# Kernel optimization log

Hardware: AMD Instinct MI355X
Metric: run time of the kernel (lower is better)

Reference implementation:

```python
import jax, jax.numpy as jnp
import numpy as np

B, T, D, H, DFF = 2, 2048, 1024, 16, 4096
DK = D // H
EPS = 1e-5


def setup_inputs() -> dict:
    key = jax.random.key(0)
    ks = jax.random.split(key, 8)
    s = 0.02
    return {
        "x": jax.random.normal(ks[0], (B, T, D), jnp.float32),
        "Wq": jax.random.normal(ks[1], (D, D), jnp.float32) * s,
        "Wk": jax.random.normal(ks[2], (D, D), jnp.float32) * s,
        "Wv": jax.random.normal(ks[3], (D, D), jnp.float32) * s,
        "Wo": jax.random.normal(ks[4], (D, D), jnp.float32) * s,
        "W1": jax.random.normal(ks[5], (DFF, D), jnp.float32) * s,
        "b1": jnp.zeros((DFF,), jnp.float32),
        "W2": jax.random.normal(ks[6], (DFF, DFF), jnp.float32) * s,
        "b2": jnp.zeros((DFF,), jnp.float32),
        "W3": jax.random.normal(ks[7], (D, DFF), jnp.float32) * s,
        "b3": jnp.zeros((D,), jnp.float32),
        "gamma1": jnp.ones((D,), jnp.float32),
        "beta1": jnp.zeros((D,), jnp.float32),
        "gamma2": jnp.ones((D,), jnp.float32),
        "beta2": jnp.zeros((D,), jnp.float32),
    }


def _layernorm(X, gamma, beta):
    X = X.astype(jnp.float32)
    mean = X.mean(axis=-1, keepdims=True)
    var = X.var(axis=-1, keepdims=True)  # unbiased=False
    X_hat = (X - mean) * jax.lax.rsqrt(var + EPS)
    return gamma * X_hat + beta


def _block(x, Wq, Wk, Wv, Wo, W1, b1, W2, b2, W3, b3, gamma1, beta1, gamma2, beta2):
    Bx, Tx, _ = x.shape
    # attention (nn.Linear: y = x @ W.T)
    Q = (x @ Wq.T).reshape(Bx, Tx, H, DK).transpose(0, 2, 1, 3)  # (B,H,T,dk)
    K = (x @ Wk.T).reshape(Bx, Tx, H, DK).transpose(0, 2, 1, 3)
    V = (x @ Wv.T).reshape(Bx, Tx, H, DK).transpose(0, 2, 1, 3)
    scores = jnp.einsum("bhqd,bhkd->bhqk", Q, K) / jnp.sqrt(jnp.float32(DK))
    causal = jnp.tril(jnp.ones((Tx, Tx), bool))
    scores = jnp.where(causal, scores, -jnp.inf)
    attn = jax.nn.softmax(scores.astype(jnp.float32), axis=-1)
    out = jnp.einsum("bhqk,bhkd->bhqd", attn, V)
    out = out.transpose(0, 2, 1, 3).reshape(Bx, Tx, D)
    attention = out @ Wo.T
    # addnorm1 (dropout=0)
    x = _layernorm(attention + x, gamma1, beta1)
    # FFN: 3 linears with exact GELU
    h = jax.nn.gelu(x @ W1.T + b1, approximate=False)
    h = jax.nn.gelu(h @ W2.T + b2, approximate=False)
    ffn_out = h @ W3.T + b3
    # addnorm2
    return _layernorm(ffn_out + x, gamma2, beta2)


def reference(x, Wq, Wk, Wv, Wo, W1, b1, W2, b2, W3, b3, gamma1, beta1, gamma2, beta2):
    return _block(x, Wq, Wk, Wv, Wo, W1, b1, W2, b2, W3, b3, gamma1, beta1, gamma2, beta2)
```

## Files before the change

### kernel.cpp

```cpp
#include <hip/hip_runtime.h>
#include <hip/hip_bf16.h>


#define B_   2
#define T_   2048
#define D_   1024
#define H_   16
#define DK_  64
#define DFF_ 4096
#define M_   (B_ * T_)

using short8 = __attribute__((ext_vector_type(8))) short;
using f32x4  = __attribute__((ext_vector_type(4))) float;
using us4    = __attribute__((ext_vector_type(4))) unsigned short;

__device__ __forceinline__ unsigned short f2bf(float f) {
  unsigned u = __float_as_uint(f);
  u += 0x7FFFu + ((u >> 16) & 1u);
  return (unsigned short)(u >> 16);
}

#define GLDS16(g, l)                                                      \
  __builtin_amdgcn_global_load_lds(                                       \
      (const __attribute__((address_space(1))) unsigned int*)(g),         \
      (__attribute__((address_space(3))) unsigned int*)(l), 16, 0, 0)

__global__ __launch_bounds__(256) void f2bf_k(const float* __restrict__ in,
                                              unsigned short* __restrict__ out,
                                              int n4) {
  int i = blockIdx.x * 256 + threadIdx.x;
  const int stride = gridDim.x * 256;
  for (; i < n4; i += stride) {
    const float4 v = ((const float4*)in)[i];
    us4 o;
    o[0] = f2bf(v.x); o[1] = f2bf(v.y); o[2] = f2bf(v.z); o[3] = f2bf(v.w);
    ((us4*)out)[i] = o;
  }
}

template <int MODE>
__global__ __launch_bounds__(256) void gemm_bt(
    const unsigned short* __restrict__ A, const unsigned short* __restrict__ Bw,
    const float* __restrict__ bias, const float* __restrict__ res,
    void* __restrict__ outp, int N, int K) {
  __shared__ unsigned short lA[128 * 32];
  __shared__ unsigned short lB[128 * 32];
  const int tid  = threadIdx.x;
  const int lane = tid & 63;
  const int wave = tid >> 6;
  const int row0 = blockIdx.y << 7;
  const int col0 = blockIdx.x << 7;
  const int wr = (wave >> 1) << 6;
  const int wc = (wave & 1) << 6;
  const int r  = lane & 15;
  const int c8 = (lane >> 4) << 3;

  const f32x4 z4 = {0.f, 0.f, 0.f, 0.f};
  f32x4 acc[4][4];
#pragma unroll
  for (int m = 0; m < 4; ++m)
#pragma unroll
    for (int n = 0; n < 4; ++n) acc[m][n] = z4;

  const unsigned short* gA = A + (size_t)(row0 + (tid >> 2)) * K + (tid & 3) * 8;
  const unsigned short* gB = Bw + (size_t)(col0 + (tid >> 2)) * K + (tid & 3) * 8;
  const size_t rstep = (size_t)64 * K;
  unsigned short* lAd = lA + tid * 8;
  unsigned short* lBd = lB + tid * 8;

  for (int kt = 0; kt < K; kt += 32) {
    GLDS16(gA + kt,         lAd);
    GLDS16(gA + kt + rstep, lAd + 2048);
    GLDS16(gB + kt,         lBd);
    GLDS16(gB + kt + rstep, lBd + 2048);
    __syncthreads();
    short8 af[4], bf[4];
#pragma unroll
    for (int m = 0; m < 4; ++m)
      af[m] = *(const short8*)&lA[(wr + m * 16 + r) * 32 + c8];
#pragma unroll
    for (int n = 0; n < 4; ++n)
      bf[n] = *(const short8*)&lB[(wc + n * 16 + r) * 32 + c8];
#pragma unroll
    for (int m = 0; m < 4; ++m)
#pragma unroll
      for (int n = 0; n < 4; ++n)
        acc[m][n] = __builtin_amdgcn_mfma_f32_16x16x32_bf16(af[m], bf[n],
                                                            acc[m][n], 0, 0, 0);
    __syncthreads();
  }

#pragma unroll
  for (int m = 0; m < 4; ++m) {
    const int gr0 = row0 + wr + m * 16 + ((lane >> 4) << 2);
#pragma unroll
    for (int n = 0; n < 4; ++n) {
      const int gc = col0 + wc + n * 16 + r;
#pragma unroll
      for (int j = 0; j < 4; ++j) {
        const int gr = gr0 + j;
        float v = acc[m][n][j];
        if (MODE == 0) {
          const int b = gr >> 11, t = gr & (T_ - 1);
          const int h = gc >> 6, d = gc & 63;
          ((unsigned short*)outp)[(((size_t)(b * H_ + h) * T_ + t) << 6) + d] =
              f2bf(v);
        } else if (MODE == 1) {
          const size_t o = (size_t)gr * N + gc;
          ((float*)outp)[o] = v + res[o];
        } else if (MODE == 2) {
          float xv = v + bias[gc];
          float g  = 0.5f * xv * (1.f + erff(xv * 0.70710678118654752f));
          ((unsigned short*)outp)[(size_t)gr * N + gc] = f2bf(g);
        } else {
          const size_t o = (size_t)gr * N + gc;
          ((float*)outp)[o] = v + bias[gc] + res[o];
        }
      }
    }
  }
}

__device__ __forceinline__ int swzK(int row, int col) {
  return row * 64 + (col ^ ((row & 7) << 3));
}
__device__ __forceinline__ int swzV(int row, int col) {
  return row * 64 + (col ^ (((row ^ (row >> 3)) & 7) << 3));
}

__global__ __launch_bounds__(256) void attn_k(
    const unsigned short* __restrict__ Q, const unsigned short* __restrict__ Kp,
    const unsigned short* __restrict__ Vp, unsigned short* __restrict__ O) {
  const int bh = blockIdx.y;
  const int qt = gridDim.x - 1 - blockIdx.x;
  const int q0 = qt << 6;
  const size_t base = (size_t)bh * T_ * DK_;
  const unsigned short* Qb = Q + base;
  const unsigned short* Kb = Kp + base;
  const unsigned short* Vb = Vp + base;
  const int tid = threadIdx.x, lane = tid & 63, wave = tid >> 6;
  const int r = lane & 15, c8 = (lane >> 4) << 3;

  __shared__ unsigned short lK[64 * 64];
  __shared__ unsigned short lV[64 * 64];
  __shared__ unsigned short lP[64 * 64];

  const short8 qf0 = *(const short8*)&Qb[(size_t)(q0 + wave * 16 + r) * 64 + c8];
  const short8 qf1 = *(const short8*)&Qb[(size_t)(q0 + wave * 16 + r) * 64 + 32 + c8];

  const f32x4 z4 = {0.f, 0.f, 0.f, 0.f};
  f32x4 o[4];
#pragma unroll
  for (int n = 0; n < 4; ++n) o[n] = z4;
  float mrow[4], lrow[4];
#pragma unroll
  for (int j = 0; j < 4; ++j) { mrow[j] = -1e30f; lrow[j] = 0.f; }

  const int kr = tid >> 3;
  const int kc = ((tid & 7) * 8) ^ ((kr & 7) << 3);
  const int vc = (tid & 7) * 8;

  for (int kt = 0; kt <= qt; ++kt) {
    __syncthreads();
    GLDS16(&Kb[((size_t)kt * 64 + kr) * 64 + kc],      lK + tid * 8);
    GLDS16(&Kb[((size_t)kt * 64 + 32 + kr) * 64 + kc], lK + 2048 + tid * 8);
    const short8 v0 = *(const short8*)&Vb[((size_t)kt * 64 + kr) * 64 + vc];
    const short8 v1 = *(const short8*)&Vb[((size_t)kt * 64 + 32 + kr) * 64 + vc];
#pragma unroll
    for (int e = 0; e < 8; ++e) {
      const int d0 = vc + e;
      lV[swzV(d0, kr)]      = (unsigned short)v0[e];
      lV[swzV(d0, kr + 32)] = (unsigned short)v1[e];
    }
    __syncthreads();

    f32x4 s[4];
#pragma unroll
    for (int n = 0; n < 4; ++n) {
      const int krow = n * 16 + r;
      const short8 k0 = *(const short8*)&lK[swzK(krow, c8)];
      const short8 k1 = *(const short8*)&lK[swzK(krow, c8 + 32)];
      f32x4 z = z4;
      z = __builtin_amdgcn_mfma_f32_16x16x32_bf16(qf0, k0, z, 0, 0, 0);
      z = __builtin_amdgcn_mfma_f32_16x16x32_bf16(qf1, k1, z, 0, 0, 0);
      s[n] = z;
    }

    const bool diag = (kt == qt);
#pragma unroll
    for (int n = 0; n < 4; ++n)
#pragma unroll
      for (int j = 0; j < 4; ++j) {
        float sv = s[n][j] * 0.125f;
        if (diag) {
          const int kk = n * 16 + r;
          const int qq = wave * 16 + ((lane >> 4) << 2) + j;
          if (kk > qq) sv = -1e30f;
        }
        s[n][j] = sv;
      }

#pragma unroll
    for (int j = 0; j < 4; ++j) {
      float mx = fmaxf(fmaxf(s[0][j], s[1][j]), fmaxf(s[2][j], s[3][j]));
#pragma unroll
      for (int msk = 1; msk < 16; msk <<= 1) mx = fmaxf(mx, __shfl_xor(mx, msk));
      const float mnew = fmaxf(mrow[j], mx);
      const float c = __expf(mrow[j] - mnew);
      mrow[j] = mnew;
      float rs = 0.f;
#pragma unroll
      for (int n = 0; n < 4; ++n) {
        const float p = __expf(s[n][j] - mnew);
        s[n][j] = p;
        rs += p;
      }
#pragma unroll
      for (int msk = 1; msk < 16; msk <<= 1) rs += __shfl_xor(rs, msk);
      lrow[j] = lrow[j] * c + rs;
#pragma unroll
      for (int n = 0; n < 4; ++n) o[n][j] *= c;
    }

#pragma unroll
    for (int n = 0; n < 4; ++n)
#pragma unroll
      for (int j = 0; j < 4; ++j) {
        const int q  = ((lane >> 4) << 2) + j;
        const int kk = n * 16 + r;
        lP[wave * 1024 + swzK(q, kk)] = f2bf(s[n][j]);
      }
    asm volatile("s_waitcnt lgkmcnt(0)" ::: "memory");

    const short8 pa0 = *(const short8*)&lP[wave * 1024 + swzK(r, c8)];
    const short8 pa1 = *(const short8*)&lP[wave * 1024 + swzK(r, c8 + 32)];
#pragma unroll
    for (int n = 0; n < 4; ++n) {
      const int dr = n * 16 + r;
      const short8 vb0 = *(const short8*)&lV[swzV(dr, c8)];
      const short8 vb1 = *(const short8*)&lV[swzV(dr, c8 + 32)];
      o[n] = __builtin_amdgcn_mfma_f32_16x16x32_bf16(pa0, vb0, o[n], 0, 0, 0);
      o[n] = __builtin_amdgcn_mfma_f32_16x16x32_bf16(pa1, vb1, o[n], 0, 0, 0);
    }
  }

  const int b = bh >> 4, h = bh & 15;
  float rinv[4];
#pragma unroll
  for (int j = 0; j < 4; ++j) rinv[j] = 1.f / lrow[j];
#pragma unroll
  for (int n = 0; n < 4; ++n)
#pragma unroll
    for (int j = 0; j < 4; ++j) {
      const int q = q0 + wave * 16 + ((lane >> 4) << 2) + j;
      const int d = n * 16 + r;
      O[((size_t)(b * T_ + q) * D_) + h * 64 + d] = f2bf(o[n][j] * rinv[j]);
    }
}

__global__ __launch_bounds__(256) void ln_k(const float* __restrict__ in,
                                            const float* __restrict__ gam,
                                            const float* __restrict__ bet,
                                            float* __restrict__ o32,
                                            unsigned short* __restrict__ obf) {
  const int row = blockIdx.x;
  const int tid = threadIdx.x, lane = tid & 63, wave = tid >> 6;
  const float4 v = ((const float4*)(in + (size_t)row * D_))[tid];
  __shared__ float sm[8];
  float s = v.x + v.y + v.z + v.w;
#pragma unroll
  for (int m = 32; m >= 1; m >>= 1) s += __shfl_xor(s, m);
  if (lane == 0) sm[wave] = s;
  __syncthreads();
  const float mean = (sm[0] + sm[1] + sm[2] + sm[3]) * (1.f / 1024.f);
  const float dx = v.x - mean, dy = v.y - mean, dz = v.z - mean, dw = v.w - mean;
  float q = dx * dx + dy * dy + dz * dz + dw * dw;
#pragma unroll
  for (int m = 32; m >= 1; m >>= 1) q += __shfl_xor(q, m);
  if (lane == 0) sm[4 + wave] = q;
  __syncthreads();
  const float var = (sm[4] + sm[5] + sm[6] + sm[7]) * (1.f / 1024.f);
  const float inv = rsqrtf(var + 1e-5f);
  const float4 g = ((const float4*)gam)[tid];
  const float4 b = ((const float4*)bet)[tid];
  float4 y;
  y.x = dx * inv * g.x + b.x;
  y.y = dy * inv * g.y + b.y;
  y.z = dz * inv * g.z + b.z;
  y.w = dw * inv * g.w + b.w;
  ((float4*)(o32 + (size_t)row * D_))[tid] = y;
  if (obf) {
    us4 o;
    o[0] = f2bf(y.x); o[1] = f2bf(y.y); o[2] = f2bf(y.z); o[3] = f2bf(y.w);
    ((us4*)(obf + (size_t)row * D_))[tid] = o;
  }
}

#define MB(x) ((size_t)(x) << 20)

extern "C" void kernel_launch(void* const* d_in, const int* in_sizes, int n_in,
                              void* d_out, int out_size, void* d_ws,
                              size_t ws_size, hipStream_t stream) {
  const float* x   = (const float*)d_in[0];
  const float* Wq  = (const float*)d_in[1];
  const float* Wk  = (const float*)d_in[2];
  const float* Wv  = (const float*)d_in[3];
  const float* Wo  = (const float*)d_in[4];
  const float* W1  = (const float*)d_in[5];
  const float* b1  = (const float*)d_in[6];
  const float* W2  = (const float*)d_in[7];
  const float* b2  = (const float*)d_in[8];
  const float* W3  = (const float*)d_in[9];
  const float* b3  = (const float*)d_in[10];
  const float* g1  = (const float*)d_in[11];
  const float* be1 = (const float*)d_in[12];
  const float* g2  = (const float*)d_in[13];
  const float* be2 = (const float*)d_in[14];
  float* out = (float*)d_out;

  char* w = (char*)d_ws;
  unsigned short* Wq_bf = (unsigned short*)(w + MB(0));
  unsigned short* Wk_bf = (unsigned short*)(w + MB(2));
  unsigned short* Wv_bf = (unsigned short*)(w + MB(4));
  unsigned short* Wo_bf = (unsigned short*)(w + MB(6));
  unsigned short* W1_bf = (unsigned short*)(w + MB(8));
  unsigned short* W2_bf = (unsigned short*)(w + MB(16));
  unsigned short* W3_bf = (unsigned short*)(w + MB(48));
  unsigned short* x_bf  = (unsigned short*)(w + MB(56));
  unsigned short* q_bf  = (unsigned short*)(w + MB(64));
  unsigned short* k_bf  = (unsigned short*)(w + MB(72));
  unsigned short* v_bf  = (unsigned short*)(w + MB(80));
  unsigned short* a_bf  = (unsigned short*)(w + MB(88));
  float*          res1  = (float*)(w + MB(96));
  float*          ln1f  = (float*)(w + MB(120));
  unsigned short* ln1bf = (unsigned short*)(w + MB(136));
  unsigned short* h1_bf = (unsigned short*)(w + MB(56));
  unsigned short* h2_bf = (unsigned short*)(w + MB(88));
  float*          res2  = (float*)(w + MB(56));

  auto cvt = [&](const float* src, unsigned short* dst, int n) {
    const int n4 = n >> 2;
    int blocks = (n4 + 255) / 256;
    if (blocks > 2048) blocks = 2048;
    f2bf_k<<<dim3(blocks), dim3(256), 0, stream>>>(src, dst, n4);
  };
  cvt(x,  x_bf,  M_ * D_);
  cvt(Wq, Wq_bf, D_ * D_);
  cvt(Wk, Wk_bf, D_ * D_);
  cvt(Wv, Wv_bf, D_ * D_);
  cvt(Wo, Wo_bf, D_ * D_);
  cvt(W1, W1_bf, DFF_ * D_);
  cvt(W2, W2_bf, DFF_ * DFF_);
  cvt(W3, W3_bf, D_ * DFF_);

  const dim3 blk(256);
  const dim3 gD(D_ / 128, M_ / 128);
  const dim3 gF(DFF_ / 128, M_ / 128);

  gemm_bt<0><<<gD, blk, 0, stream>>>(x_bf, Wq_bf, nullptr, nullptr, q_bf, D_, D_);
  gemm_bt<0><<<gD, blk, 0, stream>>>(x_bf, Wk_bf, nullptr, nullptr, k_bf, D_, D_);
  gemm_bt<0><<<gD, blk, 0, stream>>>(x_bf, Wv_bf, nullptr, nullptr, v_bf, D_, D_);

  attn_k<<<dim3(T_ / 64, B_ * H_), blk, 0, stream>>>(q_bf, k_bf, v_bf, a_bf);

  gemm_bt<1><<<gD, blk, 0, stream>>>(a_bf, Wo_bf, nullptr, x, res1, D_, D_);
  ln_k<<<dim3(M_), blk, 0, stream>>>(res1, g1, be1, ln1f, ln1bf);

  gemm_bt<2><<<gF, blk, 0, stream>>>(ln1bf, W1_bf, b1, nullptr, h1_bf, DFF_, D_);
  gemm_bt<2><<<gF, blk, 0, stream>>>(h1_bf, W2_bf, b2, nullptr, h2_bf, DFF_, DFF_);
  gemm_bt<3><<<gD, blk, 0, stream>>>(h2_bf, W3_bf, b3, ln1f, res2, D_, DFF_);

  ln_k<<<dim3(M_), blk, 0, stream>>>(res2, g2, be2, out, nullptr);
}
```

Baseline: 811.2 us.

## Rewrite GEMMs with 256x256 pipelined tiles, fuse QKV, split-K W3, widen attention tiles

Most of the pipeline is replaced. The eight conversion launches become one kernel, and Q/K/V are fused into a single GEMM over concatenated weights. The FFN GEMMs move to a new 512-thread 256x256-tile kernel that double-buffers LDS and uses explicit waitcnt, barriers and priority scheduling. The W3 GEMM is split along K into four partial buffers that a separate kernel sums together with bias and residual. Attention now processes 128-key tiles and uses exp2 with a prescaled log2e factor, cutting loop iterations and barrier overhead at the cost of more LDS and extra partial-sum memory traffic.

```diff
diff --git a/kernel.cpp b/kernel.cpp
--- a/kernel.cpp
+++ b/kernel.cpp
@@ -19,59 +19,221 @@
   u += 0x7FFFu + ((u >> 16) & 1u);
   return (unsigned short)(u >> 16);
 }
+__device__ __forceinline__ us4 pack4(float4 v) {
+  us4 o; o[0] = f2bf(v.x); o[1] = f2bf(v.y); o[2] = f2bf(v.z); o[3] = f2bf(v.w);
+  return o;
+}
 
 #define GLDS16(g, l)                                                      \
   __builtin_amdgcn_global_load_lds(                                       \
       (const __attribute__((address_space(1))) unsigned int*)(g),         \
       (__attribute__((address_space(3))) unsigned int*)(l), 16, 0, 0)
 
-__global__ __launch_bounds__(256) void f2bf_k(const float* __restrict__ in,
-                                              unsigned short* __restrict__ out,
-                                              int n4) {
+#define SB   __builtin_amdgcn_s_barrier()
+#define LG0  do { asm volatile("s_waitcnt lgkmcnt(0)" ::: "memory"); \
+                  __builtin_amdgcn_sched_barrier(0); } while (0)
+#define VMW2 do { asm volatile("s_waitcnt vmcnt(2)" ::: "memory");   \
+                  __builtin_amdgcn_sched_barrier(0); } while (0)
+#define VMW0 do { asm volatile("s_waitcnt vmcnt(0)" ::: "memory");   \
+                  __builtin_amdgcn_sched_barrier(0); } while (0)
+#define PR1  __builtin_amdgcn_s_setprio(1)
+#define PR0  __builtin_amdgcn_s_setprio(0)
+
+__global__ __launch_bounds__(256) void cvt_all(
+    const float* __restrict__ x,  const float* __restrict__ wq,
+    const float* __restrict__ wk, const float* __restrict__ wv,
+    const float* __restrict__ wo, const float* __restrict__ w1,
+    const float* __restrict__ w2, const float* __restrict__ w3,
+    us4* __restrict__ xb, us4* __restrict__ qkvw, us4* __restrict__ wob,
+    us4* __restrict__ w1b, us4* __restrict__ w2b, us4* __restrict__ w3b) {
   int i = blockIdx.x * 256 + threadIdx.x;
   const int stride = gridDim.x * 256;
-  for (; i < n4; i += stride) {
-    const float4 v = ((const float4*)in)[i];
-    us4 o;
-    o[0] = f2bf(v.x); o[1] = f2bf(v.y); o[2] = f2bf(v.z); o[3] = f2bf(v.w);
-    ((us4*)out)[i] = o;
+  for (; i < 8388608; i += stride) {
+    const float4* s; us4* d; int off;
+    if      (i < 1048576) { s = (const float4*)x;  d = xb;            off = i; }
+    else if (i < 1310720) { s = (const float4*)wq; d = qkvw;          off = i - 1048576; }
+    else if (i < 1572864) { s = (const float4*)wk; d = qkvw + 262144; off = i - 1310720; }
+    else if (i < 1835008) { s = (const float4*)wv; d = qkvw + 524288; off = i - 1572864; }
+    else if (i < 2097152) { s = (const float4*)wo; d = wob;           off = i - 1835008; }
+    else if (i < 3145728) { s = (const float4*)w1; d = w1b;           off = i - 2097152; }
+    else if (i < 7340032) { s = (const float4*)w2; d = w2b;           off = i - 3145728; }
+    else                  { s = (const float4*)w3; d = w3b;           off = i - 7340032; }
+    d[off] = pack4(s[off]);
   }
 }
 
 template <int MODE>
+__global__ __launch_bounds__(512, 2) void gemm8p(
+    const unsigned short* __restrict__ A, const unsigned short* __restrict__ Bw,
+    const float* __restrict__ bias, unsigned short* __restrict__ oq,
+    unsigned short* __restrict__ ok, unsigned short* __restrict__ ov,
+    float* __restrict__ pLo, float* __restrict__ pHi,
+    int N, int ldk, int klen) {
+  extern __shared__ unsigned short sm[];
+  unsigned short* lA = sm;
+  unsigned short* lB = sm + 32768;
+  const int tid = threadIdx.x, lane = tid & 63, w = tid >> 6;
+  const int wm = w >> 2, wn = w & 3;
+  const int wnlo = (wn & 1) * 64, wnhi = wn >> 1;
+  const int r16 = lane & 15, c8a = (lane >> 4) << 3;
+  const int row0 = blockIdx.y << 8, col0 = blockIdx.x << 8;
+  const int kb = (MODE == 4) ? blockIdx.z * klen : 0;
+
+  const int srow = tid >> 3;
+  const int scol = ((tid & 7) * 8) ^ ((srow & 7) << 3);
+  const size_t off0 = (size_t)srow * ldk + scol;
+  const size_t off1 = (size_t)(srow + 64) * ldk + scol;
+
+  auto stA = [&](int kt, int h) {
+    const unsigned short* g =
+        A + (size_t)(row0 + h * 128) * ldk + kb + (size_t)kt * 64;
+    unsigned short* d = lA + ((kt & 1) * 2 + h) * 8192;
+    GLDS16(g + off0, d + tid * 8);
+    GLDS16(g + off1, d + 4096 + tid * 8);
+  };
+  auto stB = [&](int kt, int h) {
+    const unsigned short* g =
+        Bw + (size_t)(col0 + h * 128) * ldk + kb + (size_t)kt * 64;
+    unsigned short* d = lB + ((kt & 1) * 2 + h) * 8192;
+    GLDS16(g + off0, d + tid * 8);
+    GLDS16(g + off1, d + 4096 + tid * 8);
+  };
+
+  f32x4 acc[8][4];
+#pragma unroll
+  for (int m = 0; m < 8; ++m)
+#pragma unroll
+    for (int n = 0; n < 4; ++n) acc[m][n] = (f32x4){0.f, 0.f, 0.f, 0.f};
+
+  short8 aR[4][2], bR[2][2];
+
+#define LDA4(DB, MQ)                                                         \
+  do {                                                                       \
+    _Pragma("unroll") for (int mf_ = 0; mf_ < 4; ++mf_) {                    \
+      const int rr = (MQ)*64 + mf_ * 16 + r16;                               \
+      const int bb = ((DB)*2 + wm) * 8192 + rr * 64;                         \
+      const int sw = (rr & 7) << 3;                                          \
+      aR[mf_][0] = *(const short8*)&lA[bb + (c8a ^ sw)];                     \
+      aR[mf_][1] = *(const short8*)&lA[bb + ((c8a + 32) ^ sw)];              \
+    }                                                                        \
+  } while (0)
+#define LDB2(DB, NP)                                                         \
+  do {                                                                       \
+    _Pragma("unroll") for (int nf_ = 0; nf_ < 2; ++nf_) {                    \
+      const int rr = wnlo + ((NP)*2 + nf_) * 16 + r16;                       \
+      const int bb = ((DB)*2 + wnhi) * 8192 + rr * 64;                       \
+      const int sw = (rr & 7) << 3;                                          \
+      bR[nf_][0] = *(const short8*)&lB[bb + (c8a ^ sw)];                     \
+      bR[nf_][1] = *(const short8*)&lB[bb + ((c8a + 32) ^ sw)];              \
+    }                                                                        \
+  } while (0)
+#define MMQ(MQ, NP)                                                          \
+  do {                                                                       \
+    _Pragma("unroll") for (int mf_ = 0; mf_ < 4; ++mf_)                      \
+    _Pragma("unroll") for (int nf_ = 0; nf_ < 2; ++nf_) {                    \
+      f32x4 c_ = acc[(MQ)*4 + mf_][(NP)*2 + nf_];                            \
+      c_ = __builtin_amdgcn_mfma_f32_16x16x32_bf16(aR[mf_][0], bR[nf_][0],   \
+                                                   c_, 0, 0, 0);             \
+      c_ = __builtin_amdgcn_mfma_f32_16x16x32_bf16(aR[mf_][1], bR[nf_][1],   \
+                                                   c_, 0, 0, 0);             \
+      acc[(MQ)*4 + mf_][(NP)*2 + nf_] = c_;                                  \
+    }                                                                        \
+  } while (0)
+#define TAIL(MQ, NP) SB; LG0; PR1; MMQ(MQ, NP); PR0; SB
+
+  const int nkt = klen >> 6;
+  stA(0, 0); stA(0, 1); stB(0, 0); stB(0, 1);
+
+  for (int i = 0; i < nkt; i += 2) {
+    stA(i + 1, 0);
+    VMW2;
+    SB;
+    LDA4(0, 0); LDB2(0, 0);
+    TAIL(0, 0);
+    stA(i + 1, 1);
+    LDB2(0, 1);
+    TAIL(0, 1);
+    stB(i + 1, 0);
+    LDA4(0, 1);
+    TAIL(1, 1);
+    stB(i + 1, 1);
+    LDB2(0, 0);
+    TAIL(1, 0);
+    const bool more = (i + 2 < nkt);
+    if (more) { stA(i + 2, 0); VMW2; } else { VMW0; }
+    SB;
+    LDA4(1, 0); LDB2(1, 0);
+    TAIL(0, 0);
+    if (more) stA(i + 2, 1);
+    LDB2(1, 1);
+    TAIL(0, 1);
+    if (more) stB(i + 2, 0);
+    LDA4(1, 1);
+    TAIL(1, 1);
+    if (more) stB(i + 2, 1);
+    LDB2(1, 0);
+    TAIL(1, 0);
+  }
+
+#pragma unroll
+  for (int am = 0; am < 8; ++am) {
+    const int gr0 = row0 + wm * 128 + am * 16 + ((lane >> 4) << 2);
+#pragma unroll
+    for (int an = 0; an < 4; ++an) {
+      const int gc = col0 + wn * 64 + an * 16 + r16;
+#pragma unroll
+      for (int j = 0; j < 4; ++j) {
+        const int gr = gr0 + j;
+        float v = acc[am][an][j];
+        if (MODE == 0) {
+          const int which = gc >> 10, c1 = gc & 1023;
+          const int b = gr >> 11, t = gr & (T_ - 1);
+          const int h = c1 >> 6, d = c1 & 63;
+          unsigned short* dst = (which == 0) ? oq : (which == 1) ? ok : ov;
+          dst[(((size_t)(b * H_ + h) * T_ + t) << 6) + d] = f2bf(v);
+        } else if (MODE == 2) {
+          float xv = v + bias[gc];
+          float g  = 0.5f * xv * (1.f + erff(xv * 0.70710678118654752f));
+          oq[(size_t)gr * N + gc] = f2bf(g);
+        } else {
+          const int z = blockIdx.z;
+          float* o = (z < 2) ? pLo + (size_t)z * (M_ * 1024)
+                             : pHi + (size_t)(z - 2) * (M_ * 1024);
+          o[(size_t)gr * 1024 + gc] = v;
+        }
+      }
+    }
+  }
+#undef LDA4
+#undef LDB2
+#undef MMQ
+#undef TAIL
+}
+
 __global__ __launch_bounds__(256) void gemm_bt(
     const unsigned short* __restrict__ A, const unsigned short* __restrict__ Bw,
-    const float* __restrict__ bias, const float* __restrict__ res,
-    void* __restrict__ outp, int N, int K) {
+    const float* __restrict__ res, float* __restrict__ outp, int N, int K) {
   __shared__ unsigned short lA[128 * 32];
   __shared__ unsigned short lB[128 * 32];
-  const int tid  = threadIdx.x;
-  const int lane = tid & 63;
-  const int wave = tid >> 6;
-  const int row0 = blockIdx.y << 7;
-  const int col0 = blockIdx.x << 7;
-  const int wr = (wave >> 1) << 6;
-  const int wc = (wave & 1) << 6;
-  const int r  = lane & 15;
-  const int c8 = (lane >> 4) << 3;
-
+  const int tid = threadIdx.x, lane = tid & 63, wave = tid >> 6;
+  const int row0 = blockIdx.y << 7, col0 = blockIdx.x << 7;
+  const int wr = (wave >> 1) << 6, wc = (wave & 1) << 6;
+  const int r = lane & 15, c8 = (lane >> 4) << 3;
   const f32x4 z4 = {0.f, 0.f, 0.f, 0.f};
   f32x4 acc[4][4];
 #pragma unroll
   for (int m = 0; m < 4; ++m)
 #pragma unroll
     for (int n = 0; n < 4; ++n) acc[m][n] = z4;
-
   const unsigned short* gA = A + (size_t)(row0 + (tid >> 2)) * K + (tid & 3) * 8;
   const unsigned short* gB = Bw + (size_t)(col0 + (tid >> 2)) * K + (tid & 3) * 8;
   const size_t rstep = (size_t)64 * K;
   unsigned short* lAd = lA + tid * 8;
   unsigned short* lBd = lB + tid * 8;
-
   for (int kt = 0; kt < K; kt += 32) {
-    GLDS16(gA + kt,         lAd);
+    GLDS16(gA + kt, lAd);
     GLDS16(gA + kt + rstep, lAd + 2048);
-    GLDS16(gB + kt,         lBd);
+    GLDS16(gB + kt, lBd);
     GLDS16(gB + kt + rstep, lBd + 2048);
     __syncthreads();
     short8 af[4], bf[4];
@@ -89,7 +251,6 @@
                                                             acc[m][n], 0, 0, 0);
     __syncthreads();
   }
-
 #pragma unroll
   for (int m = 0; m < 4; ++m) {
     const int gr0 = row0 + wr + m * 16 + ((lane >> 4) << 2);
@@ -98,34 +259,11 @@
       const int gc = col0 + wc + n * 16 + r;
 #pragma unroll
       for (int j = 0; j < 4; ++j) {
-        const int gr = gr0 + j;
-        float v = acc[m][n][j];
-        if (MODE == 0) {
-          const int b = gr >> 11, t = gr & (T_ - 1);
-          const int h = gc >> 6, d = gc & 63;
-          ((unsigned short*)outp)[(((size_t)(b * H_ + h) * T_ + t) << 6) + d] =
-              f2bf(v);
-        } else if (MODE == 1) {
-          const size_t o = (size_t)gr * N + gc;
-          ((float*)outp)[o] = v + res[o];
-        } else if (MODE == 2) {
-          float xv = v + bias[gc];
-          float g  = 0.5f * xv * (1.f + erff(xv * 0.70710678118654752f));
-          ((unsigned short*)outp)[(size_t)gr * N + gc] = f2bf(g);
-        } else {
-          const size_t o = (size_t)gr * N + gc;
-          ((float*)outp)[o] = v + bias[gc] + res[o];
-        }
-      }
-    }
-  }
-}
-
-__device__ __forceinline__ int swzK(int row, int col) {
-  return row * 64 + (col ^ ((row & 7) << 3));
-}
-__device__ __forceinline__ int swzV(int row, int col) {
-  return row * 64 + (col ^ (((row ^ (row >> 3)) & 7) << 3));
+        const size_t o = (size_t)(gr0 + j) * N + gc;
+        outp[o] = acc[m][n][j] + res[o];
+      }
+    }
+  }
 }
 
 __global__ __launch_bounds__(256) void attn_k(
@@ -141,12 +279,13 @@
   const int tid = threadIdx.x, lane = tid & 63, wave = tid >> 6;
   const int r = lane & 15, c8 = (lane >> 4) << 3;
 
-  __shared__ unsigned short lK[64 * 64];
-  __shared__ unsigned short lV[64 * 64];
-  __shared__ unsigned short lP[64 * 64];
+  __shared__ unsigned short lK[128 * 64];
+  __shared__ unsigned short lV[64 * 128];
+  __shared__ unsigned short lP[4 * 16 * 128];
 
   const short8 qf0 = *(const short8*)&Qb[(size_t)(q0 + wave * 16 + r) * 64 + c8];
-  const short8 qf1 = *(const short8*)&Qb[(size_t)(q0 + wave * 16 + r) * 64 + 32 + c8];
+  const short8 qf1 =
+      *(const short8*)&Qb[(size_t)(q0 + wave * 16 + r) * 64 + 32 + c8];
 
   const f32x4 z4 = {0.f, 0.f, 0.f, 0.f};
   f32x4 o[4];
@@ -156,63 +295,75 @@
 #pragma unroll
   for (int j = 0; j < 4; ++j) { mrow[j] = -1e30f; lrow[j] = 0.f; }
 
-  const int kr = tid >> 3;
-  const int kc = ((tid & 7) * 8) ^ ((kr & 7) << 3);
-  const int vc = (tid & 7) * 8;
-
-  for (int kt = 0; kt <= qt; ++kt) {
+  const float SCL = 0.125f * 1.44269504088896f;
+  const int krow = tid >> 3;
+  const int kcol = ((tid & 7) * 8) ^ ((krow & 7) << 3);
+
+  const int niter = (q0 >> 7) + 1;
+  for (int kt = 0; kt < niter; ++kt) {
     __syncthreads();
-    GLDS16(&Kb[((size_t)kt * 64 + kr) * 64 + kc],      lK + tid * 8);
-    GLDS16(&Kb[((size_t)kt * 64 + 32 + kr) * 64 + kc], lK + 2048 + tid * 8);
-    const short8 v0 = *(const short8*)&Vb[((size_t)kt * 64 + kr) * 64 + vc];
-    const short8 v1 = *(const short8*)&Vb[((size_t)kt * 64 + 32 + kr) * 64 + vc];
-#pragma unroll
-    for (int e = 0; e < 8; ++e) {
-      const int d0 = vc + e;
-      lV[swzV(d0, kr)]      = (unsigned short)v0[e];
-      lV[swzV(d0, kr + 32)] = (unsigned short)v1[e];
-    }
+    const unsigned short* Kt = Kb + ((size_t)kt << 7) * 64;
+    GLDS16(Kt + krow * 64 + kcol,         lK + tid * 8);
+    GLDS16(Kt + (krow + 32) * 64 + kcol,  lK + 2048 + tid * 8);
+    GLDS16(Kt + (krow + 64) * 64 + kcol,  lK + 4096 + tid * 8);
+    GLDS16(Kt + (krow + 96) * 64 + kcol,  lK + 6144 + tid * 8);
+    const unsigned short* Vt = Vb + ((size_t)kt << 7) * 64;
+    short8 vld[4];
+#pragma unroll
+    for (int l = 0; l < 4; ++l)
+      vld[l] = *(const short8*)&Vt[(size_t)((tid >> 3) + 32 * l) * 64 +
+                                   (tid & 7) * 8];
+#pragma unroll
+    for (int l = 0; l < 4; ++l)
+#pragma unroll
+      for (int e = 0; e < 8; ++e) {
+        const int dd = (tid & 7) * 8 + e, kv = (tid >> 3) + 32 * l;
+        lV[dd * 128 + (kv ^ ((dd & 7) << 3))] = (unsigned short)vld[l][e];
+      }
     __syncthreads();
 
-    f32x4 s[4];
-#pragma unroll
-    for (int n = 0; n < 4; ++n) {
-      const int krow = n * 16 + r;
-      const short8 k0 = *(const short8*)&lK[swzK(krow, c8)];
-      const short8 k1 = *(const short8*)&lK[swzK(krow, c8 + 32)];
+    f32x4 s[8];
+#pragma unroll
+    for (int nf = 0; nf < 8; ++nf) {
+      const int kr = nf * 16 + r;
+      const int sw = (kr & 7) << 3;
+      const short8 k0 = *(const short8*)&lK[kr * 64 + (c8 ^ sw)];
+      const short8 k1 = *(const short8*)&lK[kr * 64 + ((c8 + 32) ^ sw)];
       f32x4 z = z4;
       z = __builtin_amdgcn_mfma_f32_16x16x32_bf16(qf0, k0, z, 0, 0, 0);
       z = __builtin_amdgcn_mfma_f32_16x16x32_bf16(qf1, k1, z, 0, 0, 0);
-      s[n] = z;
-    }
-
-    const bool diag = (kt == qt);
-#pragma unroll
-    for (int n = 0; n < 4; ++n)
+      s[nf] = z;
+    }
+
+    const bool tail = (kt == niter - 1);
+#pragma unroll
+    for (int nf = 0; nf < 8; ++nf)
 #pragma unroll
       for (int j = 0; j < 4; ++j) {
-        float sv = s[n][j] * 0.125f;
-        if (diag) {
-          const int kk = n * 16 + r;
-          const int qq = wave * 16 + ((lane >> 4) << 2) + j;
-          if (kk > qq) sv = -1e30f;
+        float sv = s[nf][j] * SCL;
+        if (tail) {
+          const int kg = (kt << 7) + nf * 16 + r;
+          const int qg = q0 + wave * 16 + ((lane >> 4) << 2) + j;
+          if (kg > qg) sv = -1e30f;
         }
-        s[n][j] = sv;
+        s[nf][j] = sv;
       }
 
 #pragma unroll
     for (int j = 0; j < 4; ++j) {
-      float mx = fmaxf(fmaxf(s[0][j], s[1][j]), fmaxf(s[2][j], s[3][j]));
+      float mx = s[0][j];
+#pragma unroll
+      for (int nf = 1; nf < 8; ++nf) mx = fmaxf(mx, s[nf][j]);
 #pragma unroll
       for (int msk = 1; msk < 16; msk <<= 1) mx = fmaxf(mx, __shfl_xor(mx, msk));
       const float mnew = fmaxf(mrow[j], mx);
-      const float c = __expf(mrow[j] - mnew);
+      const float c = exp2f(mrow[j] - mnew);
       mrow[j] = mnew;
       float rs = 0.f;
 #pragma unroll
-      for (int n = 0; n < 4; ++n) {
-        const float p = __expf(s[n][j] - mnew);
-        s[n][j] = p;
+      for (int nf = 0; nf < 8; ++nf) {
+        const float p = exp2f(s[nf][j] - mnew);
+        s[nf][j] = p;
         rs += p;
       }
 #pragma unroll
@@ -222,25 +373,34 @@
       for (int n = 0; n < 4; ++n) o[n][j] *= c;
     }
 
-#pragma unroll
-    for (int n = 0; n < 4; ++n)
+    unsigned short* Pw = lP + wave * 2048;
+#pragma unroll
+    for (int nf = 0; nf < 8; ++nf)
 #pragma unroll
       for (int j = 0; j < 4; ++j) {
-        const int q  = ((lane >> 4) << 2) + j;
-        const int kk = n * 16 + r;
-        lP[wave * 1024 + swzK(q, kk)] = f2bf(s[n][j]);
+        const int q = ((lane >> 4) << 2) + j, kk = nf * 16 + r;
+        Pw[q * 128 + (kk ^ ((q & 7) << 3))] = f2bf(s[nf][j]);
       }
     asm volatile("s_waitcnt lgkmcnt(0)" ::: "memory");
-
-    const short8 pa0 = *(const short8*)&lP[wave * 1024 + swzK(r, c8)];
-    const short8 pa1 = *(const short8*)&lP[wave * 1024 + swzK(r, c8 + 32)];
-#pragma unroll
-    for (int n = 0; n < 4; ++n) {
-      const int dr = n * 16 + r;
-      const short8 vb0 = *(const short8*)&lV[swzV(dr, c8)];
-      const short8 vb1 = *(const short8*)&lV[swzV(dr, c8 + 32)];
-      o[n] = __builtin_amdgcn_mfma_f32_16x16x32_bf16(pa0, vb0, o[n], 0, 0, 0);
-      o[n] = __builtin_amdgcn_mfma_f32_16x16x32_bf16(pa1, vb1, o[n], 0, 0, 0);
+    __builtin_amdgcn_sched_barrier(0);
+
+    short8 pa[4];
+#pragma unroll
+    for (int kh = 0; kh < 4; ++kh) {
+      const int cc = kh * 32 + c8;
+      pa[kh] = *(const short8*)&Pw[r * 128 + (cc ^ ((r & 7) << 3))];
+    }
+#pragma unroll
+    for (int df = 0; df < 4; ++df) {
+      const int dr = df * 16 + r;
+      const int sw = (dr & 7) << 3;
+#pragma unroll
+      for (int kh = 0; kh < 4; ++kh) {
+        const int cc = kh * 32 + c8;
+        const short8 vb = *(const short8*)&lV[dr * 128 + (cc ^ sw)];
+        o[df] = __builtin_amdgcn_mfma_f32_16x16x32_bf16(pa[kh], vb, o[df],
+                                                        0, 0, 0);
+      }
     }
   }
 
@@ -256,6 +416,25 @@
       const int d = n * 16 + r;
       O[((size_t)(b * T_ + q) * D_) + h * 64 + d] = f2bf(o[n][j] * rinv[j]);
     }
+}
+
+__global__ __launch_bounds__(256) void red_k(
+    const float4* __restrict__ p0, const float4* __restrict__ p1,
+    const float4* __restrict__ p2, const float4* __restrict__ p3,
+    const float4* __restrict__ ln1, const float4* __restrict__ b3,
+    float4* __restrict__ res2) {
+  int i = blockIdx.x * 256 + threadIdx.x;
+  const int stride = gridDim.x * 256;
+  for (; i < M_ * 256; i += stride) {
+    const float4 a = p0[i], b = p1[i], c = p2[i], d = p3[i], e = ln1[i];
+    const float4 bb = b3[i & 255];
+    float4 v;
+    v.x = a.x + b.x + c.x + d.x + e.x + bb.x;
+    v.y = a.y + b.y + c.y + d.y + e.y + bb.y;
+    v.z = a.z + b.z + c.z + d.z + e.z + bb.z;
+    v.w = a.w + b.w + c.w + d.w + e.w + bb.w;
+    res2[i] = v;
+  }
 }
 
 __global__ __launch_bounds__(256) void ln_k(const float* __restrict__ in,
@@ -319,56 +498,60 @@
   float* out = (float*)d_out;
 
   char* w = (char*)d_ws;
-  unsigned short* Wq_bf = (unsigned short*)(w + MB(0));
-  unsigned short* Wk_bf = (unsigned short*)(w + MB(2));
-  unsigned short* Wv_bf = (unsigned short*)(w + MB(4));
-  unsigned short* Wo_bf = (unsigned short*)(w + MB(6));
-  unsigned short* W1_bf = (unsigned short*)(w + MB(8));
-  unsigned short* W2_bf = (unsigned short*)(w + MB(16));
-  unsigned short* W3_bf = (unsigned short*)(w + MB(48));
-  unsigned short* x_bf  = (unsigned short*)(w + MB(56));
+  unsigned short* x_bf  = (unsigned short*)(w + MB(0));
+  unsigned short* qkvw  = (unsigned short*)(w + MB(8));
+  unsigned short* Wo_bf = (unsigned short*)(w + MB(14));
+  unsigned short* W1_bf = (unsigned short*)(w + MB(16));
+  unsigned short* W2_bf = (unsigned short*)(w + MB(24));
+  unsigned short* W3_bf = (unsigned short*)(w + MB(56));
   unsigned short* q_bf  = (unsigned short*)(w + MB(64));
   unsigned short* k_bf  = (unsigned short*)(w + MB(72));
   unsigned short* v_bf  = (unsigned short*)(w + MB(80));
   unsigned short* a_bf  = (unsigned short*)(w + MB(88));
-  float*          res1  = (float*)(w + MB(96));
-  float*          ln1f  = (float*)(w + MB(120));
-  unsigned short* ln1bf = (unsigned short*)(w + MB(136));
-  unsigned short* h1_bf = (unsigned short*)(w + MB(56));
-  unsigned short* h2_bf = (unsigned short*)(w + MB(88));
-  float*          res2  = (float*)(w + MB(56));
-
-  auto cvt = [&](const float* src, unsigned short* dst, int n) {
-    const int n4 = n >> 2;
-    int blocks = (n4 + 255) / 256;
-    if (blocks > 2048) blocks = 2048;
-    f2bf_k<<<dim3(blocks), dim3(256), 0, stream>>>(src, dst, n4);
-  };
-  cvt(x,  x_bf,  M_ * D_);
-  cvt(Wq, Wq_bf, D_ * D_);
-  cvt(Wk, Wk_bf, D_ * D_);
-  cvt(Wv, Wv_bf, D_ * D_);
-  cvt(Wo, Wo_bf, D_ * D_);
-  cvt(W1, W1_bf, DFF_ * D_);
-  cvt(W2, W2_bf, DFF_ * DFF_);
-  cvt(W3, W3_bf, D_ * DFF_);
-
-  const dim3 blk(256);
-  const dim3 gD(D_ / 128, M_ / 128);
-  const dim3 gF(DFF_ / 128, M_ / 128);
-
-  gemm_bt<0><<<gD, blk, 0, stream>>>(x_bf, Wq_bf, nullptr, nullptr, q_bf, D_, D_);
-  gemm_bt<0><<<gD, blk, 0, stream>>>(x_bf, Wk_bf, nullptr, nullptr, k_bf, D_, D_);
-  gemm_bt<0><<<gD, blk, 0, stream>>>(x_bf, Wv_bf, nullptr, nullptr, v_bf, D_, D_);
-
-  attn_k<<<dim3(T_ / 64, B_ * H_), blk, 0, stream>>>(q_bf, k_bf, v_bf, a_bf);
-
-  gemm_bt<1><<<gD, blk, 0, stream>>>(a_bf, Wo_bf, nullptr, x, res1, D_, D_);
-  ln_k<<<dim3(M_), blk, 0, stream>>>(res1, g1, be1, ln1f, ln1bf);
-
-  gemm_bt<2><<<gF, blk, 0, stream>>>(ln1bf, W1_bf, b1, nullptr, h1_bf, DFF_, D_);
-  gemm_bt<2><<<gF, blk, 0, stream>>>(h1_bf, W2_bf, b2, nullptr, h2_bf, DFF_, DFF_);
-  gemm_bt<3><<<gD, blk, 0, stream>>>(h2_bf, W3_bf, b3, ln1f, res2, D_, DFF_);
-
-  ln_k<<<dim3(M_), blk, 0, stream>>>(res2, g2, be2, out, nullptr);
-}
+  float*          res1  = (float*)(w + MB(64));
+  float*          ln1f  = (float*)(w + MB(0));
+  unsigned short* ln1bf = (unsigned short*)(w + MB(128));
+  unsigned short* h1_bf = (unsigned short*)(w + MB(96));
+  unsigned short* h2_bf = (unsigned short*)(w + MB(64));
+  float*          part0 = (float*)(w + MB(16));
+  float*          part2 = (float*)(w + MB(96));
+  float*          res2  = (float*)(w + MB(80));
+
+  (void)hipFuncSetAttribute((const void*)gemm8p<0>,
+      hipFuncAttributeMaxDynamicSharedMemorySize, 131072);
+  (void)hipFuncSetAttribute((const void*)gemm8p<2>,
+      hipFuncAttributeMaxDynamicSharedMemorySize, 131072);
+  (void)hipFuncSetAttribute((const void*)gemm8p<4>,
+      hipFuncAttributeMaxDynamicSharedMemorySize, 131072);
+
+  cvt_all<<<dim3(2048), dim3(256), 0, stream>>>(
+      x, Wq, Wk, Wv, Wo, W1, W2, W3, (us4*)x_bf, (us4*)qkvw, (us4*)Wo_bf,
+      (us4*)W1_bf, (us4*)W2_bf, (us4*)W3_bf);
+
+  gemm8p<0><<<dim3(12, 16), dim3(512), 131072, stream>>>(
+      x_bf, qkvw, nullptr, q_bf, k_bf, v_bf, nullptr, nullptr,
+      3072, 1024, 1024);
+
+  attn_k<<<dim3(T_ / 64, B_ * H_), dim3(256), 0, stream>>>(q_bf, k_bf, v_bf,
+                                                           a_bf);
+
+  gemm_bt<<<dim3(8, 32), dim3(256), 0, stream>>>(a_bf, Wo_bf, x, res1, D_, D_);
+  ln_k<<<dim3(M_), dim3(256), 0, stream>>>(res1, g1, be1, ln1f, ln1bf);
+
+  gemm8p<2><<<dim3(16, 16), dim3(512), 131072, stream>>>(
+      ln1bf, W1_bf, b1, h1_bf, nullptr, nullptr, nullptr, nullptr,
+      DFF_, 1024, 1024);
+  gemm8p<2><<<dim3(16, 16), dim3(512), 131072, stream>>>(
+      h1_bf, W2_bf, b2, h2_bf, nullptr, nullptr, nullptr, nullptr,
+      DFF_, 4096, 4096);
+  gemm8p<4><<<dim3(4, 16, 4), dim3(512), 131072, stream>>>(
+      h2_bf, W3_bf, nullptr, nullptr, nullptr, nullptr, part0, part2,
+      D_, 4096, 1024);
+
+  red_k<<<dim3(2048), dim3(256), 0, stream>>>(
+      (const float4*)part0, (const float4*)(w + MB(32)),
+      (const float4*)part2, (const float4*)(w + MB(112)),
+      (const float4*)ln1f, (const float4*)b3, (float4*)res2);
+
+  ln_k<<<dim3(M_), dim3(256), 0, stream>>>(res2, g2, be2, out, nullptr);
+}
```

Result: faster. 649.8 us (-19.9%).
